# Performance work log

Hardware: AMD Instinct MI355X
Metric: run time of the kernel (lower is better)

The kernel has to match this reference:

```python
import jax, jax.numpy as jnp
import numpy as np
from jax import lax

B, T, U, V, D, H = 4, 256, 64, 1024, 256, 256
BLANK = V - 1
NEG = -1.0e30
CTC_W = 0.3


def setup_inputs():
    ks = jax.random.split(jax.random.key(0), 9)
    return {
        "x_enc": jax.random.normal(ks[0], (B, T, D), jnp.float32),
        "x_dec": jax.random.normal(ks[1], (B, U + 1, H), jnp.float32),
        "W_enc": jax.random.normal(ks[2], (D, H), jnp.float32) / float(np.sqrt(D)),
        "b_enc": jnp.zeros((H,), jnp.float32),
        "W_dec": jax.random.normal(ks[3], (H, H), jnp.float32) / float(np.sqrt(H)),
        "b_dec": jnp.zeros((H,), jnp.float32),
        "W_out": jax.random.normal(ks[4], (H, V), jnp.float32) / float(np.sqrt(H)),
        "b_out": jnp.zeros((V,), jnp.float32),
        "W_ctc": jax.random.normal(ks[5], (D, V), jnp.float32) / float(np.sqrt(D)),
        "b_ctc": jnp.zeros((V,), jnp.float32),
        "target": jax.random.randint(ks[6], (B, U), 0, V - 1, jnp.int32),
        "frame_length": (T - jax.random.randint(ks[7], (B,), 0, T // 4)).astype(jnp.int32),
        "target_length": (U - jax.random.randint(ks[8], (B,), 0, U // 4)).astype(jnp.int32),
    }


def _forward(x_enc, x_dec, W_enc, b_enc, W_dec, b_dec, W_out, b_out, W_ctc, b_ctc,
             target, frame_length, target_length):
    b_idx = jnp.arange(B)
    ft, tl = frame_length, target_length

    # ---- Joiner: broadcast-add of projected enc/pred states, tanh, output proj ----
    h = jnp.tanh((x_enc @ W_enc + b_enc)[:, :, None, :]
                 + (x_dec @ W_dec + b_dec)[:, None, :, :])        # [B,T,U+1,H]
    logp = jax.nn.log_softmax(h @ W_out + b_out, axis=-1)          # [B,T,U+1,V]

    # gather=True trick: only blank and target-label log-probs are needed
    lp_blank = logp[..., BLANK]                                    # [B,T,U+1]
    lp_label = jnp.take_along_axis(
        logp[:, :, :U, :],
        jnp.broadcast_to(target[:, None, :, None], (B, T, U, 1)), axis=3)[..., 0]  # [B,T,U]

    # ---- RNNT forward DP over the (T, U+1) lattice ----
    def u_scan(b0, lbl):
        # b0[u] = alpha[t-1,u] + blank[t-1,u]; alpha[t,u] = logaddexp(b0[u], alpha[t,u-1]+lbl[u-1])
        def step(c, xs):
            bu, lu = xs
            new = jnp.logaddexp(bu, c + lu)
            return new, new
        _, outs = lax.scan(step, b0[:, 0],
                           (jnp.moveaxis(b0[:, 1:], 1, 0), jnp.moveaxis(lbl, 1, 0)))
        return jnp.concatenate([b0[:, :1], jnp.moveaxis(outs, 0, 1)], axis=1)

    alpha0 = jnp.concatenate([jnp.zeros((B, 1), logp.dtype),
                              jnp.cumsum(lp_label[:, 0, :], axis=1)], axis=1)  # [B,U+1]

    def t_step(prev, xs):
        blk_prev, lbl_t = xs
        a = u_scan(prev + blk_prev, lbl_t)
        return a, a

    _, rest = lax.scan(t_step, alpha0,
                       (jnp.moveaxis(lp_blank[:, :-1, :], 1, 0),
                        jnp.moveaxis(lp_label[:, 1:, :], 1, 0)))
    alphas = jnp.concatenate([alpha0[None], rest], axis=0)          # [T,B,U+1]
    ll = alphas[ft - 1, b_idx, tl] + lp_blank[b_idx, ft - 1, tl]
    rnnt_loss = jnp.mean(-ll)

    # ---- CTC branch: linear head on encoder output + standard CTC DP ----
    logp_ctc = jax.nn.log_softmax(x_enc @ W_ctc + b_ctc, axis=-1)   # [B,T,V]
    S = 2 * U + 1
    ext = jnp.full((B, S), BLANK, jnp.int32).at[:, 1::2].set(target)
    emit = jnp.take_along_axis(logp_ctc,
                               jnp.broadcast_to(ext[:, None, :], (B, T, S)), axis=2)  # [B,T,S]
    skip = jnp.concatenate([jnp.zeros((B, 2), bool),
                            (ext[:, 2:] != BLANK) & (ext[:, 2:] != ext[:, :-2])], axis=1)
    c0 = jnp.full((B, S), NEG, logp_ctc.dtype).at[:, 0].set(emit[:, 0, 0]).at[:, 1].set(emit[:, 0, 1])

    def c_step(prev, xs):
        emit_t, t = xs
        p2 = jnp.concatenate([jnp.full((B, 1), NEG, prev.dtype), prev[:, :-1]], axis=1)
        p3 = jnp.where(skip,
                       jnp.concatenate([jnp.full((B, 2), NEG, prev.dtype), prev[:, :-2]], axis=1),
                       NEG)
        new = emit_t + jnp.logaddexp(jnp.logaddexp(prev, p2), p3)
        new = jnp.where((t < ft)[:, None], new, prev)  # freeze past frame_length
        return new, None

    cT, _ = lax.scan(c_step, c0, (jnp.moveaxis(emit[:, 1:, :], 1, 0), jnp.arange(1, T)))
    s_last = 2 * tl
    ll_ctc = jnp.logaddexp(cT[b_idx, s_last], cT[b_idx, s_last - 1])
    ctc_loss = jnp.where(ll_ctc < NEG / 2, 0.0, -ll_ctc).sum() / B  # zero_infinity, sum/B

    return rnnt_loss + CTC_W * ctc_loss


def reference(x_enc, x_dec, W_enc, b_enc, W_dec, b_dec, W_out, b_out, W_ctc, b_ctc,
              target, frame_length, target_length):
    return _forward(x_enc, x_dec, W_enc, b_enc, W_dec, b_dec, W_out, b_out, W_ctc, b_ctc,
                    target, frame_length, target_length)
```

## Files before the change

kernel.cpp:

```cpp
#include <hip/hip_runtime.h>
#include <hip/hip_bf16.h>

#define Bn 4
#define Tn 256
#define Un 64
#define UP1 65
#define Vn 1024
#define Dn 256
#define Hn 256
#define BLANKC 1023
#define NEGF (-1.0e30f)
#define CTCW 0.3f
#define R2E 1.4426950408889634f
#define LN2 0.6931471805599453f

typedef __attribute__((ext_vector_type(8))) short short8;
typedef __attribute__((ext_vector_type(4))) float f32x4;
typedef __attribute__((ext_vector_type(4))) unsigned int u32x4;

static __device__ __forceinline__ unsigned short f2bf(float f) {
  unsigned int u = __float_as_uint(f);
  u += 0x7FFFu + ((u >> 16) & 1u);
  return (unsigned short)(u >> 16);
}
static __device__ __forceinline__ unsigned int pack2bf(float a, float b) {
  return (unsigned int)f2bf(a) | ((unsigned int)f2bf(b) << 16);
}
static __device__ __forceinline__ float ftanh(float x) {
  float e = __expf(2.0f * x);
  return 1.0f - 2.0f / (e + 1.0f);
}
static __device__ __forceinline__ float ex2(float x) {
  return __builtin_amdgcn_exp2f(x);
}
static __device__ __forceinline__ float lg2(float x) {
  return __builtin_amdgcn_logf(x);
}
static __device__ __forceinline__ float laddexp2_(float x, float y) {
  float m = fmaxf(x, y);
  float d = y - x;
  return m + lg2(1.0f + ex2(-fabsf(d)));
}
static __device__ __forceinline__ float laddexp3_2(float a, float b, float c) {
  float m = fmaxf(fmaxf(a, b), c);
  return m + lg2(ex2(a - m) + ex2(b - m) + ex2(c - m));
}
static __device__ __forceinline__ float shfl_up1(float x) {
  int r = __builtin_amdgcn_update_dpp(0, __float_as_int(x), 0x138, 0xF, 0xF, false);
  return __int_as_float(r);
}

__global__ __launch_bounds__(256) void k_prep(
    const float* __restrict__ W_enc, const float* __restrict__ W_dec,
    const float* __restrict__ W_out, const float* __restrict__ W_ctc,
    unsigned short* __restrict__ Wt_enc, unsigned short* __restrict__ Wt_dec,
    unsigned short* __restrict__ Wt_out, unsigned short* __restrict__ Wt_ctc,
    float* __restrict__ out) {
  const int blk = blockIdx.x, tid = threadIdx.x;
  if (blk == 0 && tid == 0) out[0] = 0.0f;
  __shared__ float tilebuf[64][65];
  if (blk < 128) {
    const float* Wsrc = (blk < 64) ? W_out : W_ctc;
    unsigned short* Wd = (blk < 64) ? Wt_out : Wt_ctc;
    const int tt = blk & 63;
    const int k0 = (tt & 3) * 64, v0 = (tt >> 2) * 64;
#pragma unroll
    for (int rep = 0; rep < 16; ++rep) {
      int e = rep * 256 + tid;
      int rr = e >> 6, cc = e & 63;
      tilebuf[rr][cc] = Wsrc[(k0 + rr) * 1024 + (v0 + cc)];
    }
    __syncthreads();
#pragma unroll
    for (int rep = 0; rep < 16; ++rep) {
      int e = rep * 256 + tid;
      int nn = e >> 6, kk = e & 63;
      int n = v0 + nn, k = k0 + kk;
      int c = n >> 8, col = n & 255;
      int ks = k >> 5, sub = (k >> 3) & 3, k7 = k & 7;
      Wd[(c * 8 + ks) * 8192 + sub * 2048 + col * 8 + k7] = f2bf(tilebuf[kk][nn]);
    }
  } else {
    const float* Wsrc = (blk < 144) ? W_enc : W_dec;
    unsigned short* Wd = (blk < 144) ? Wt_enc : Wt_dec;
    const int tt = (blk - 128) & 15;
    const int k0 = (tt & 3) * 64, v0 = (tt >> 2) * 64;
#pragma unroll
    for (int rep = 0; rep < 16; ++rep) {
      int e = rep * 256 + tid;
      int rr = e >> 6, cc = e & 63;
      tilebuf[rr][cc] = Wsrc[(k0 + rr) * 256 + (v0 + cc)];
    }
    __syncthreads();
#pragma unroll
    for (int rep = 0; rep < 16; ++rep) {
      int e = rep * 256 + tid;
      int rr = e >> 6, cc = e & 63;
      Wd[(v0 + rr) * 256 + (k0 + cc)] = f2bf(tilebuf[cc][rr]);
    }
  }
}

__global__ __launch_bounds__(256) void k_lin(
    const float* __restrict__ x_enc, const float* __restrict__ x_dec,
    const unsigned short* __restrict__ Wt_enc, const float* __restrict__ b_enc,
    const unsigned short* __restrict__ Wt_dec, const float* __restrict__ b_dec,
    float* __restrict__ enc_lin, float* __restrict__ dec_lin) {
  __shared__ __align__(16) char Asw[64 * 512];
  const int tid = threadIdx.x;
  const int w = tid >> 6, l = tid & 63;
  const int l15 = l & 15, l4 = l >> 4;
  const bool enc = blockIdx.x < 16;
  const int m0 = enc ? blockIdx.x * 64 : (blockIdx.x - 16) * 64;
  const int Mlim = enc ? 1024 : 260;
  const float* xp = enc ? x_enc : x_dec;
  const unsigned short* Wt = enc ? Wt_enc : Wt_dec;
  const float* bias = enc ? b_enc : b_dec;
  float* outp = enc ? enc_lin : dec_lin;

#pragma unroll
  for (int it = 0; it < 8; ++it) {
    int e = (it << 8) + tid;
    int i = e >> 5;
    int k0 = (e & 31) << 3;
    int r = m0 + i;
    if (r > Mlim - 1) r = Mlim - 1;
    const float* sp = xp + r * 256 + k0;
    f32x4 e0 = *(const f32x4*)sp;
    f32x4 e1 = *(const f32x4*)(sp + 4);
    u32x4 pv;
    pv[0] = pack2bf(e0[0], e0[1]);
    pv[1] = pack2bf(e0[2], e0[3]);
    pv[2] = pack2bf(e1[0], e1[1]);
    pv[3] = pack2bf(e1[2], e1[3]);
    int byt = (i << 9) + (k0 << 1);
    byt ^= (i & 7) << 4;
    *(u32x4*)(Asw + byt) = pv;
  }
  __syncthreads();

  const int nb = w * 64;
  f32x4 acc[4][4] = {};
#pragma unroll
  for (int ks = 0; ks < 8; ++ks) {
    int k = ks * 32 + l4 * 8;
    short8 af[4];
#pragma unroll
    for (int mt = 0; mt < 4; ++mt) {
      int i = mt * 16 + l15;
      int byt = (i << 9) + (k << 1);
      byt ^= (i & 7) << 4;
      af[mt] = *(const short8*)(Asw + byt);
    }
    short8 bfr[4];
#pragma unroll
    for (int nt = 0; nt < 4; ++nt) {
      int n = nb + nt * 16 + l15;
      bfr[nt] = *(const short8*)(Wt + n * 256 + k);
    }
#pragma unroll
    for (int mt = 0; mt < 4; ++mt)
#pragma unroll
      for (int nt = 0; nt < 4; ++nt)
        acc[mt][nt] = __builtin_amdgcn_mfma_f32_16x16x32_bf16(
            af[mt], bfr[nt], acc[mt][nt], 0, 0, 0);
  }
  float biasv[4];
#pragma unroll
  for (int nt = 0; nt < 4; ++nt) biasv[nt] = bias[nb + nt * 16 + l15];
#pragma unroll
  for (int mt = 0; mt < 4; ++mt)
#pragma unroll
    for (int rr = 0; rr < 4; ++rr) {
      int row = m0 + mt * 16 + l4 * 4 + rr;
      if (row < Mlim) {
#pragma unroll
        for (int nt = 0; nt < 4; ++nt)
          outp[row * 256 + nb + nt * 16 + l15] = acc[mt][nt][rr] + biasv[nt];
      }
    }
}

__global__ __launch_bounds__(256) void k_join2(
    const float* __restrict__ enc_lin, const float* __restrict__ dec_lin,
    const unsigned short* __restrict__ Wt_out, const float* __restrict__ b_out,
    const float* __restrict__ x_enc,
    const unsigned short* __restrict__ Wt_ctc, const float* __restrict__ b_ctc,
    const int* __restrict__ target,
    float* __restrict__ lp_blank, float* __restrict__ lp_label,
    float* __restrict__ ctc_blank, float* __restrict__ ctc_lse,
    float* __restrict__ ctc_lab) {
  __shared__ __align__(16) char Asw[64 * 512];
  __shared__ float s_psum[4][64];
  __shared__ float s_blank[64], s_label[64];
  __shared__ int s_tgt[64];

  const int tid = threadIdx.x;
  const int w = tid >> 6, l = tid & 63;
  const int l15 = l & 15, l4 = l >> 4;
  const int bid = blockIdx.x;

  const bool joiner = bid >= 16;
  const unsigned short* Wt = joiner ? Wt_out : Wt_ctc;
  const float* bias = joiner ? b_out : b_ctc;

  const unsigned short* tb = Wt + l4 * 2048 + (w * 64 + l15) * 8;

  short8 bE[4], bO[4];
#define LOADB(REG, S)                                                          \
  {                                                                            \
    const unsigned short* p_ = tb + (S)*8192;                                  \
    _Pragma("unroll") for (int nt = 0; nt < 4; ++nt)                           \
        REG[nt] = *(const short8*)(p_ + nt * 128);                             \
  }
  {
    const int sc0 = (bid & 3) * 8;
    LOADB(bE, sc0 + 0)
    LOADB(bO, sc0 + 1)
  }

  int b, r0 = 0, g0 = 0;
  if (joiner) {
    const int jbid = bid - 16;
    b = jbid / 260;
    r0 = (jbid % 260) * 64;
#pragma unroll
    for (int it = 0; it < 8; ++it) {
      int e = (it << 8) + tid;
      int i = e >> 5;
      int k0 = (e & 31) << 3;
      int r = r0 + i;
      int t = r / 65;
      int u = r - t * 65;
      const float* ep = enc_lin + ((b * Tn + t) * Hn + k0);
      const float* dp = dec_lin + ((b * UP1 + u) * Hn + k0);
      f32x4 e0 = *(const f32x4*)ep;
      f32x4 e1 = *(const f32x4*)(ep + 4);
      f32x4 d0 = *(const f32x4*)dp;
      f32x4 d1 = *(const f32x4*)(dp + 4);
      u32x4 pv;
      pv[0] = pack2bf(ftanh(e0[0] + d0[0]) * R2E, ftanh(e0[1] + d0[1]) * R2E);
      pv[1] = pack2bf(ftanh(e0[2] + d0[2]) * R2E, ftanh(e0[3] + d0[3]) * R2E);
      pv[2] = pack2bf(ftanh(e1[0] + d1[0]) * R2E, ftanh(e1[1] + d1[1]) * R2E);
      pv[3] = pack2bf(ftanh(e1[2] + d1[2]) * R2E, ftanh(e1[3] + d1[3]) * R2E);
      int byt = (i << 9) + (k0 << 1);
      byt ^= (i & 7) << 4;
      *(u32x4*)(Asw + byt) = pv;
    }
    if (tid < 64) {
      int u = (r0 + tid) % 65;
      s_tgt[tid] = (u < Un) ? target[b * Un + u] : -1;
    }
  } else {
    g0 = bid * 64;
    b = g0 >> 8;
#pragma unroll
    for (int it = 0; it < 8; ++it) {
      int e = (it << 8) + tid;
      int i = e >> 5;
      int k0 = (e & 31) << 3;
      const float* sp = x_enc + (g0 + i) * Dn + k0;
      f32x4 e0 = *(const f32x4*)sp;
      f32x4 e1 = *(const f32x4*)(sp + 4);
      u32x4 pv;
      pv[0] = pack2bf(e0[0] * R2E, e0[1] * R2E);
      pv[1] = pack2bf(e0[2] * R2E, e0[3] * R2E);
      pv[2] = pack2bf(e1[0] * R2E, e1[1] * R2E);
      pv[3] = pack2bf(e1[2] * R2E, e1[3] * R2E);
      int byt = (i << 9) + (k0 << 1);
      byt ^= (i & 7) << 4;
      *(u32x4*)(Asw + byt) = pv;
    }
    if (tid < 64) s_tgt[tid] = target[b * Un + tid];
  }
  __syncthreads();

  float ssum[16];
#pragma unroll
  for (int j = 0; j < 16; ++j) ssum[j] = 0.0f;

#define MFMASTEP(REG, KS)                                                      \
  {                                                                            \
    const int k_ = (KS)*32 + l4 * 8;                                           \
    _Pragma("unroll") for (int mt = 0; mt < 4; ++mt) {                         \
      int i_ = mt * 16 + l15;                                                  \
      int byt_ = ((i_ << 9) + (k_ << 1)) ^ ((i_ & 7) << 4);                    \
      short8 af_ = *(const short8*)(Asw + byt_);                               \
      _Pragma("unroll") for (int nt = 0; nt < 4; ++nt)                         \
          acc[mt][nt] = __builtin_amdgcn_mfma_f32_16x16x32_bf16(               \
              af_, REG[nt], acc[mt][nt], 0, 0, 0);                             \
    }                                                                          \
  }
#define SB __builtin_amdgcn_sched_barrier(0)

#pragma unroll 1
  for (int cr = 0; cr < 4; ++cr) {
    const int cc = (cr + bid) & 3;
    const int sc = cc * 8;
    const int scn = ((cr + 1 + bid) & 3) * 8;
    f32x4 acc[4][4] = {};
    MFMASTEP(bE, 0) LOADB(bE, sc + 2) SB;
    MFMASTEP(bO, 1) LOADB(bO, sc + 3) SB;
    MFMASTEP(bE, 2) LOADB(bE, sc + 4) SB;
    MFMASTEP(bO, 3) LOADB(bO, sc + 5) SB;
    MFMASTEP(bE, 4) LOADB(bE, sc + 6) SB;
    MFMASTEP(bO, 5) LOADB(bO, sc + 7) SB;
    MFMASTEP(bE, 6) LOADB(bE, (cr < 3) ? scn + 0 : sc + 6) SB;
    MFMASTEP(bO, 7) LOADB(bO, (cr < 3) ? scn + 1 : sc + 7) SB;

    const int nb = cc * 256 + w * 64;
    float biasv[4];
#pragma unroll
    for (int nt = 0; nt < 4; ++nt) biasv[nt] = bias[nb + nt * 16 + l15] * R2E;
#pragma unroll
    for (int mt = 0; mt < 4; ++mt)
#pragma unroll
      for (int nt = 0; nt < 4; ++nt)
#pragma unroll
        for (int rr = 0; rr < 4; ++rr) acc[mt][nt][rr] += biasv[nt];

    if (joiner) {
      if (cc == 3 && w == 3 && l15 == 15) {
#pragma unroll
        for (int mt = 0; mt < 4; ++mt)
#pragma unroll
          for (int rr = 0; rr < 4; ++rr)
            s_blank[mt * 16 + l4 * 4 + rr] = acc[mt][3][rr];
      }
#pragma unroll
      for (int mt = 0; mt < 4; ++mt)
#pragma unroll
        for (int rr = 0; rr < 4; ++rr) {
          int row = mt * 16 + l4 * 4 + rr;
          int tg = s_tgt[row];
          if ((tg >> 8) == cc && ((tg >> 6) & 3) == w && (tg & 15) == l15) {
            int ntv = (tg >> 4) & 3;
            float v01 = (ntv & 1) ? acc[mt][1][rr] : acc[mt][0][rr];
            float v23 = (ntv & 1) ? acc[mt][3][rr] : acc[mt][2][rr];
            s_label[row] = (ntv & 2) ? v23 : v01;
          }
        }
    } else {
      if (cc == 3 && w == 3 && l15 == 15) {
#pragma unroll
        for (int mt = 0; mt < 4; ++mt)
#pragma unroll
          for (int rr = 0; rr < 4; ++rr)
            s_blank[mt * 16 + l4 * 4 + rr] = acc[mt][3][rr];
      }
#pragma unroll 1
      for (int u = 0; u < 64; ++u) {
        int tgu = s_tgt[u];
        if ((tgu >> 8) == cc && ((tgu >> 6) & 3) == w) {
          int ntv = (tgu >> 4) & 3;
          if ((tgu & 15) == l15) {
#pragma unroll
            for (int mt = 0; mt < 4; ++mt)
#pragma unroll
              for (int rr = 0; rr < 4; ++rr) {
                float v01 = (ntv & 1) ? acc[mt][1][rr] : acc[mt][0][rr];
                float v23 = (ntv & 1) ? acc[mt][3][rr] : acc[mt][2][rr];
                float v = (ntv & 2) ? v23 : v01;
                ctc_lab[(g0 + mt * 16 + l4 * 4 + rr) * 64 + u] = v;
              }
          }
        }
      }
    }
#pragma unroll
    for (int mt = 0; mt < 4; ++mt)
#pragma unroll
      for (int rr = 0; rr < 4; ++rr)
        ssum[mt * 4 + rr] += ex2(acc[mt][0][rr]) + ex2(acc[mt][1][rr]) +
                             ex2(acc[mt][2][rr]) + ex2(acc[mt][3][rr]);
  }
#undef MFMASTEP
#undef LOADB
#undef SB

#pragma unroll
  for (int ms = 1; ms < 16; ms <<= 1)
#pragma unroll
    for (int j = 0; j < 16; ++j) ssum[j] += __shfl_xor(ssum[j], ms, 64);
  if (l15 == 0) {
#pragma unroll
    for (int j = 0; j < 16; ++j)
      s_psum[w][(j >> 2) * 16 + l4 * 4 + (j & 3)] = ssum[j];
  }
  __syncthreads();

  if (tid < 64) {
    float tot = s_psum[0][tid] + s_psum[1][tid] + s_psum[2][tid] + s_psum[3][tid];
    float lse = lg2(tot);
    if (joiner) {
      int r = r0 + tid;
      int t = r / 65;
      int u = r - t * 65;
      lp_blank[(b * Tn + t) * UP1 + u] = s_blank[tid] - lse;
      if (u < Un) lp_label[(b * Tn + t) * Un + u] = s_label[tid] - lse;
    } else {
      ctc_blank[g0 + tid] = s_blank[tid] - lse;
      ctc_lse[g0 + tid] = lse;
    }
  }
}

__global__ __launch_bounds__(256) void k_dp(
    const float* __restrict__ lp_blank, const float* __restrict__ lp_label,
    const float* __restrict__ ctc_blank, const float* __restrict__ ctc_lse,
    const float* __restrict__ ctc_lab,
    const int* __restrict__ target,
    const int* __restrict__ flen, const int* __restrict__ tlen,
    float* __restrict__ out) {
  __shared__ float sA[256 * 66];
  __shared__ __align__(16) float sB[16384];
  __shared__ float sC[256], sD[256];
  __shared__ float cT[129];
  const int tid = threadIdx.x;
  const int l = tid & 63;

  if (blockIdx.x < 4) {
    const int b = blockIdx.x;
    for (int i = tid; i < 16640; i += 256) {
      int r = i / 65, cidx = i - r * 65;
      sA[r * 66 + cidx] = lp_blank[b * 16640 + i];
    }
    {
      const f32x4* g2 = (const f32x4*)(lp_label + b * 16384);
      f32x4* s2 = (f32x4*)sB;
      for (int i = tid; i < 4096; i += 256) s2[i] = g2[i];
    }
    __syncthreads();
    if (tid < 64) {
      const int ft = flen[b], tl = tlen[b];
      const int dstar = ft - 1 + tl;
      const bool isown = (l == tl);
      const bool is64 = (tl == 64) && (l == 63);
      const int lc = (l >= 1) ? l - 1 : 0;

#define RLOAD(D0, VB, VL, VB64, VL64)                                          \
  _Pragma("unroll") for (int j = 0; j < 8; ++j) {                              \
    const int d_ = (D0) + j;                                                   \
    const int t_ = d_ - l;                                                     \
    const int tbc_ = (t_ < 1) ? 1 : (t_ > 255 ? 255 : t_);                     \
    const int tcc_ = (t_ < 0) ? 0 : (t_ > 255 ? 255 : t_);                     \
    VB[j] = sA[(tbc_ - 1) * 66 + l];                                           \
    VL[j] = (l == 0) ? NEGF : sB[tcc_ * 64 + lc];                              \
    const int t64_ = d_ - 64;                                                  \
    const int t64b_ = (t64_ < 1) ? 1 : (t64_ > 255 ? 255 : t64_);              \
    const int t64c_ = (t64_ < 0) ? 0 : (t64_ > 255 ? 255 : t64_);              \
    VB64[j] = sA[(t64b_ - 1) * 66 + 64];                                       \
    VL64[j] = sB[t64c_ * 64 + 63];                                             \
  }

      float cvb[8], cvl[8], cvb64[8], cvl64[8];
      RLOAD(1, cvb, cvl, cvb64, cvl64);
      float a = (l == 0) ? 0.0f : NEGF;
      float a64 = NEGF, cap = NEGF;
      for (int d0 = 1; d0 <= dstar; d0 += 8) {
        float nvb[8], nvl[8], nvb64[8], nvl64[8];
        RLOAD(d0 + 8, nvb, nvl, nvb64, nvl64);
        __builtin_amdgcn_sched_barrier(0);
#pragma unroll
        for (int j = 0; j < 8; ++j) {
          const int d = d0 + j;
          float aleft = shfl_up1(a);
          float x = a + cvb[j];
          float y = aleft + cvl[j];
          float nw = laddexp2_(x, y);
          float nw64 = laddexp2_(a64 + cvb64[j], a + cvl64[j]);
          a = nw;
          a64 = (l == 63) ? nw64 : a64;
          bool hit = (d == dstar);
          cap = (hit && isown) ? a : cap;
          cap = (hit && is64) ? a64 : cap;
        }
        __builtin_amdgcn_sched_barrier(0);
#pragma unroll
        for (int j = 0; j < 8; ++j) {
          cvb[j] = nvb[j];
          cvl[j] = nvl[j];
          cvb64[j] = nvb64[j];
          cvl64[j] = nvl64[j];
        }
      }
#undef RLOAD
      bool owner = (tl < 64) ? isown : (l == 63);
      if (owner)
        atomicAdd(out, -0.25f * LN2 * (cap + sA[(ft - 1) * 66 + tl]));
    }
  } else {
    const int b = blockIdx.x - 4;
    {
      const f32x4* g2 = (const f32x4*)(ctc_lab + b * 16384);
      f32x4* s2 = (f32x4*)sB;
      for (int i = tid; i < 4096; i += 256) s2[i] = g2[i];
      sC[tid] = ctc_blank[b * 256 + tid];
      sD[tid] = ctc_lse[b * 256 + tid];
    }
    __syncthreads();
    if (tid < 64) {
      const int ft = flen[b], tl = tlen[b];
      const int tg = target[b * Un + l];
      const int tgp = (l >= 1) ? target[b * Un + l - 1] : -1;
      const bool skip1 = (l >= 1) && (tg != tgp);

#define CLOAD(T0, EB, E1)                                                      \
  _Pragma("unroll") for (int j = 0; j < 8; ++j) {                              \
    const int tc_ = ((T0) + j > 255) ? 255 : (T0) + j;                         \
    EB[j] = sC[tc_];                                                           \
    E1[j] = sB[tc_ * 64 + l] - sD[tc_];                                        \
  }

      float ceb[8], ce1[8];
      CLOAD(1, ceb, ce1);
      float a0 = (l == 0) ? sC[0] : NEGF;
      float a1 = (l == 0) ? (sB[0] - sD[0]) : NEGF;
      float a2 = NEGF;
      for (int t0 = 1; t0 < ft; t0 += 8) {
        float neb[8], ne1[8];
        CLOAD(t0 + 8, neb, ne1);
        __builtin_amdgcn_sched_barrier(0);
#pragma unroll
        for (int j = 0; j < 8; ++j) {
          const int t = t0 + j;
          float pm1 = shfl_up1(a1);
          pm1 = (l == 0) ? NEGF : pm1;
          float n0 = ceb[j] + laddexp2_(a0, pm1);
          float n1 = ce1[j] + laddexp3_2(a1, a0, skip1 ? pm1 : NEGF);
          float n2 = ceb[j] + laddexp2_(a2, a1);
          bool run = (t < ft);
          a0 = run ? n0 : a0;
          a1 = run ? n1 : a1;
          a2 = (run && (l == 63)) ? n2 : a2;
        }
        __builtin_amdgcn_sched_barrier(0);
#pragma unroll
        for (int j = 0; j < 8; ++j) {
          ceb[j] = neb[j];
          ce1[j] = ne1[j];
        }
      }
#undef CLOAD
      cT[2 * l] = a0;
      cT[2 * l + 1] = a1;
      if (l == 63) cT[128] = a2;
      __builtin_amdgcn_s_waitcnt(0);
      if (l == 0) {
        int sl = 2 * tl;
        float ll = laddexp2_(cT[sl], cT[sl - 1]);
        float lb = (ll < NEGF * 0.7f) ? 0.0f : -ll;
        atomicAdd(out, CTCW * 0.25f * LN2 * lb);
      }
    }
  }
}

extern "C" void kernel_launch(void* const* d_in, const int* in_sizes, int n_in,
                              void* d_out, int out_size, void* d_ws, size_t ws_size,
                              hipStream_t stream) {
  (void)in_sizes; (void)n_in; (void)out_size; (void)ws_size;
  const float* x_enc = (const float*)d_in[0];
  const float* x_dec = (const float*)d_in[1];
  const float* W_enc = (const float*)d_in[2];
  const float* b_enc = (const float*)d_in[3];
  const float* W_dec = (const float*)d_in[4];
  const float* b_dec = (const float*)d_in[5];
  const float* W_out = (const float*)d_in[6];
  const float* b_out = (const float*)d_in[7];
  const float* W_ctc = (const float*)d_in[8];
  const float* b_ctc = (const float*)d_in[9];
  const int* target = (const int*)d_in[10];
  const int* flen = (const int*)d_in[11];
  const int* tlen = (const int*)d_in[12];

  float* ws = (float*)d_ws;
  float* enc_lin = ws;
  float* dec_lin = ws + 262144;
  float* lp_blank = ws + 328704;
  float* lp_label = ws + 395264;
  float* ctc_blank = ws + 460800;
  float* ctc_lse = ws + 461824;
  float* ctc_lab = ws + 462848;
  unsigned short* Wt_out = (unsigned short*)(ws + 528384);
  unsigned short* Wt_ctc = Wt_out + 262144;
  unsigned short* Wt_enc = (unsigned short*)lp_blank;
  unsigned short* Wt_dec = (unsigned short*)lp_label;
  float* out = (float*)d_out;

  k_prep<<<dim3(160), dim3(256), 0, stream>>>(
      W_enc, W_dec, W_out, W_ctc, Wt_enc, Wt_dec, Wt_out, Wt_ctc, out);
  k_lin<<<dim3(21), dim3(256), 0, stream>>>(
      x_enc, x_dec, Wt_enc, b_enc, Wt_dec, b_dec, enc_lin, dec_lin);
  k_join2<<<dim3(1056), dim3(256), 0, stream>>>(
      enc_lin, dec_lin, Wt_out, b_out, x_enc, Wt_ctc, b_ctc, target,
      lp_blank, lp_label, ctc_blank, ctc_lse, ctc_lab);
  k_dp<<<dim3(8), dim3(64 * 4), 0, stream>>>(
      lp_blank, lp_label, ctc_blank, ctc_lse, ctc_lab, target, flen, tlen, out);
}
```

Before: 121.9 us.

## Shrink k_lin tiles, raise MFMA priority, specialize DP inner loops

k_lin now uses 32-row tiles and launches 41 blocks instead of 21, spreading the small projection GEMM over more CUs. The joiner MFMA steps are wrapped in s_setprio so matrix work is favored over concurrent loads. The RNNT and CTC DP loops get branch-specialized fast paths that drop the per-step capture and frame-length checks when they cannot fire. The added branching is wave-uniform, and the extra k_lin blocks re-read the B weights more often.

```diff
diff --git a/kernel.cpp b/kernel.cpp
--- a/kernel.cpp
+++ b/kernel.cpp
@@ -106,12 +106,12 @@
     const unsigned short* __restrict__ Wt_enc, const float* __restrict__ b_enc,
     const unsigned short* __restrict__ Wt_dec, const float* __restrict__ b_dec,
     float* __restrict__ enc_lin, float* __restrict__ dec_lin) {
-  __shared__ __align__(16) char Asw[64 * 512];
+  __shared__ __align__(16) char Asw[32 * 512];
   const int tid = threadIdx.x;
   const int w = tid >> 6, l = tid & 63;
   const int l15 = l & 15, l4 = l >> 4;
-  const bool enc = blockIdx.x < 16;
-  const int m0 = enc ? blockIdx.x * 64 : (blockIdx.x - 16) * 64;
+  const bool enc = blockIdx.x < 32;
+  const int m0 = enc ? blockIdx.x * 32 : (blockIdx.x - 32) * 32;
   const int Mlim = enc ? 1024 : 260;
   const float* xp = enc ? x_enc : x_dec;
   const unsigned short* Wt = enc ? Wt_enc : Wt_dec;
@@ -119,7 +119,7 @@
   float* outp = enc ? enc_lin : dec_lin;
 
 #pragma unroll
-  for (int it = 0; it < 8; ++it) {
+  for (int it = 0; it < 4; ++it) {
     int e = (it << 8) + tid;
     int i = e >> 5;
     int k0 = (e & 31) << 3;
@@ -140,13 +140,13 @@
   __syncthreads();
 
   const int nb = w * 64;
-  f32x4 acc[4][4] = {};
+  f32x4 acc[2][4] = {};
 #pragma unroll
   for (int ks = 0; ks < 8; ++ks) {
     int k = ks * 32 + l4 * 8;
-    short8 af[4];
-#pragma unroll
-    for (int mt = 0; mt < 4; ++mt) {
+    short8 af[2];
+#pragma unroll
+    for (int mt = 0; mt < 2; ++mt) {
       int i = mt * 16 + l15;
       int byt = (i << 9) + (k << 1);
       byt ^= (i & 7) << 4;
@@ -159,7 +159,7 @@
       bfr[nt] = *(const short8*)(Wt + n * 256 + k);
     }
 #pragma unroll
-    for (int mt = 0; mt < 4; ++mt)
+    for (int mt = 0; mt < 2; ++mt)
 #pragma unroll
       for (int nt = 0; nt < 4; ++nt)
         acc[mt][nt] = __builtin_amdgcn_mfma_f32_16x16x32_bf16(
@@ -169,7 +169,7 @@
 #pragma unroll
   for (int nt = 0; nt < 4; ++nt) biasv[nt] = bias[nb + nt * 16 + l15];
 #pragma unroll
-  for (int mt = 0; mt < 4; ++mt)
+  for (int mt = 0; mt < 2; ++mt)
 #pragma unroll
     for (int rr = 0; rr < 4; ++rr) {
       int row = m0 + mt * 16 + l4 * 4 + rr;
@@ -281,6 +281,7 @@
 
 #define MFMASTEP(REG, KS)                                                      \
   {                                                                            \
+    __builtin_amdgcn_s_setprio(1);                                             \
     const int k_ = (KS)*32 + l4 * 8;                                           \
     _Pragma("unroll") for (int mt = 0; mt < 4; ++mt) {                         \
       int i_ = mt * 16 + l15;                                                  \
@@ -290,6 +291,7 @@
           acc[mt][nt] = __builtin_amdgcn_mfma_f32_16x16x32_bf16(               \
               af_, REG[nt], acc[mt][nt], 0, 0, 0);                             \
     }                                                                          \
+    __builtin_amdgcn_s_setprio(0);                                             \
   }
 #define SB __builtin_amdgcn_sched_barrier(0)
 
@@ -461,19 +463,33 @@
         float nvb[8], nvl[8], nvb64[8], nvl64[8];
         RLOAD(d0 + 8, nvb, nvl, nvb64, nvl64);
         __builtin_amdgcn_sched_barrier(0);
-#pragma unroll
-        for (int j = 0; j < 8; ++j) {
-          const int d = d0 + j;
-          float aleft = shfl_up1(a);
-          float x = a + cvb[j];
-          float y = aleft + cvl[j];
-          float nw = laddexp2_(x, y);
-          float nw64 = laddexp2_(a64 + cvb64[j], a + cvl64[j]);
-          a = nw;
-          a64 = (l == 63) ? nw64 : a64;
-          bool hit = (d == dstar);
-          cap = (hit && isown) ? a : cap;
-          cap = (hit && is64) ? a64 : cap;
+        const bool hashit = ((unsigned)(dstar - d0)) < 8u;
+        if (hashit) {
+#pragma unroll
+          for (int j = 0; j < 8; ++j) {
+            const int d = d0 + j;
+            float aleft = shfl_up1(a);
+            float x = a + cvb[j];
+            float y = aleft + cvl[j];
+            float nw = laddexp2_(x, y);
+            float nw64 = laddexp2_(a64 + cvb64[j], a + cvl64[j]);
+            a = nw;
+            a64 = (l == 63) ? nw64 : a64;
+            bool hit = (d == dstar);
+            cap = (hit && isown) ? a : cap;
+            cap = (hit && is64) ? a64 : cap;
+          }
+        } else {
+#pragma unroll
+          for (int j = 0; j < 8; ++j) {
+            float aleft = shfl_up1(a);
+            float x = a + cvb[j];
+            float y = aleft + cvl[j];
+            float nw = laddexp2_(x, y);
+            float nw64 = laddexp2_(a64 + cvb64[j], a + cvl64[j]);
+            a = nw;
+            a64 = (l == 63) ? nw64 : a64;
+          }
         }
         __builtin_amdgcn_sched_barrier(0);
 #pragma unroll
@@ -521,18 +537,33 @@
         float neb[8], ne1[8];
         CLOAD(t0 + 8, neb, ne1);
         __builtin_amdgcn_sched_barrier(0);
-#pragma unroll
-        for (int j = 0; j < 8; ++j) {
-          const int t = t0 + j;
-          float pm1 = shfl_up1(a1);
-          pm1 = (l == 0) ? NEGF : pm1;
-          float n0 = ceb[j] + laddexp2_(a0, pm1);
-          float n1 = ce1[j] + laddexp3_2(a1, a0, skip1 ? pm1 : NEGF);
-          float n2 = ceb[j] + laddexp2_(a2, a1);
-          bool run = (t < ft);
-          a0 = run ? n0 : a0;
-          a1 = run ? n1 : a1;
-          a2 = (run && (l == 63)) ? n2 : a2;
+        const bool alive = (t0 + 8 <= ft);
+        if (alive) {
+#pragma unroll
+          for (int j = 0; j < 8; ++j) {
+            float pm1 = shfl_up1(a1);
+            pm1 = (l == 0) ? NEGF : pm1;
+            float n0 = ceb[j] + laddexp2_(a0, pm1);
+            float n1 = ce1[j] + laddexp3_2(a1, a0, skip1 ? pm1 : NEGF);
+            float n2 = ceb[j] + laddexp2_(a2, a1);
+            a0 = n0;
+            a1 = n1;
+            a2 = (l == 63) ? n2 : a2;
+          }
+        } else {
+#pragma unroll
+          for (int j = 0; j < 8; ++j) {
+            const int t = t0 + j;
+            float pm1 = shfl_up1(a1);
+            pm1 = (l == 0) ? NEGF : pm1;
+            float n0 = ceb[j] + laddexp2_(a0, pm1);
+            float n1 = ce1[j] + laddexp3_2(a1, a0, skip1 ? pm1 : NEGF);
+            float n2 = ceb[j] + laddexp2_(a2, a1);
+            bool run = (t < ft);
+            a0 = run ? n0 : a0;
+            a1 = run ? n1 : a1;
+            a2 = (run && (l == 63)) ? n2 : a2;
+          }
         }
         __builtin_amdgcn_sched_barrier(0);
 #pragma unroll
@@ -590,7 +621,7 @@
 
   k_prep<<<dim3(160), dim3(256), 0, stream>>>(
       W_enc, W_dec, W_out, W_ctc, Wt_enc, Wt_dec, Wt_out, Wt_ctc, out);
-  k_lin<<<dim3(21), dim3(256), 0, stream>>>(
+  k_lin<<<dim3(41), dim3(256), 0, stream>>>(
       x_enc, x_dec, Wt_enc, b_enc, Wt_dec, b_dec, enc_lin, dec_lin);
   k_join2<<<dim3(1056), dim3(256), 0, stream>>>(
       enc_lin, dec_lin, Wt_out, b_out, x_enc, Wt_ctc, b_ctc, target,
```

Result: no change. 120.3 us (-1.3%).
